# Performance work log

Hardware: AMD Instinct MI355X
Metric: run time of the kernel (lower is better)

Reference implementation:

```python
import jax, jax.numpy as jnp
import numpy as np

N_NODES = 50000
N_EDGES = 600000
D_FEAT = 128


def setup_inputs() -> dict:
    key = jax.random.key(0)
    k1, k2, k3 = jax.random.split(key, 3)
    x = jax.random.normal(k1, (N_NODES, D_FEAT), dtype=jnp.float32)
    edge_index = jax.random.randint(k2, (2, N_EDGES), 0, N_NODES, dtype=jnp.int64)
    line_graph_val = jax.random.normal(k3, (N_EDGES,), dtype=jnp.float32)  # unused by module
    return {"x": x, "edge_index": edge_index, "line_graph_val": line_graph_val}


def reference(x, edge_index, line_graph_val):
    # edge_index is unpacked as (j, i): j = source, i = target (GCN convention)
    src = edge_index[0]  # j
    dst = edge_index[1]  # i
    n = x.shape[0]
    # deg = scatter-add of ones over target indices i
    deg = jax.ops.segment_sum(jnp.ones_like(src, dtype=x.dtype), dst, num_segments=n)
    # deg^{-1/2}; guard deg==0 (torch would give inf; isolated targets have no edges anyway)
    deg_inv_sqrt = jnp.where(deg > 0, deg ** -0.5, jnp.zeros_like(deg))
    norm = deg_inv_sqrt[src] * deg_inv_sqrt[dst]  # [E]
    # spmm(edge_index[[1,0]], norm, n, n, x): out[i] += norm_e * x[j]
    msg = norm[:, None] * x[src]  # [E, F]
    out = jax.ops.segment_sum(msg, dst, num_segments=n)  # [N, F]
    return jax.nn.relu(out)
```

## Files before the change

kernel.cpp:

```cpp
#include <hip/hip_runtime.h>


#define SORTB    512
#define CHUNKMAX 1184
#define NBP      512
#define BCAP     2048

__device__ __forceinline__ int detect_is64(const unsigned int* w) {
    const int t = threadIdx.x & 63;
    unsigned long long m = __ballot(w[2 * t + 1] != 0u);
    return m == 0ull ? 1 : 0;
}

__device__ __forceinline__ int load_idx(const void* p, long long i, int is64) {
    return is64 ? (int)((const long long*)p)[i] : ((const int*)p)[i];
}

__device__ __forceinline__ unsigned short f2bf(float f) {
    unsigned u = __float_as_uint(f);
    unsigned r = (u + 0x7fffu + ((u >> 16) & 1u)) >> 16;
    return (unsigned short)r;
}

__global__ void k_zero_cur(int* cursor, int nb) {
    for (int i = threadIdx.x; i < nb; i += blockDim.x) cursor[i] = 0;
}

__global__ void __launch_bounds__(256) k_zero(int4* p, int n4) {
    const int stride = gridDim.x * blockDim.x;
    for (int i = blockIdx.x * blockDim.x + threadIdx.x; i < n4; i += stride)
        p[i] = make_int4(0, 0, 0, 0);
}


__global__ void __launch_bounds__(256) k_sort(const void* ei, int* cursor,
                                              unsigned int* __restrict__ buckets,
                                              int E, int CH) {
    __shared__ unsigned int raw[CHUNKMAX];
    __shared__ unsigned int srt[CHUNKMAX];
    __shared__ int hist[NBP];
    __shared__ int lbase[NBP];
    __shared__ int gbase[NBP];
    __shared__ int lcur[NBP];
    const int bid = blockIdx.x;
    const int t = threadIdx.x;
    for (int i = t; i < NBP; i += 256) hist[i] = 0;
    __syncthreads();
    const int is64 = detect_is64((const unsigned int*)ei);
    const int e0 = bid * CH;
    const int e1 = min(e0 + CH, E);
    const int nch = e1 - e0;
    for (int i = t; i < nch; i += 256) {
        const long long e = e0 + i;
        int s = load_idx(ei, e, is64);
        int d = load_idx(ei, (long long)E + e, is64);
        unsigned w = ((unsigned)d << 16) | (unsigned)s;
        raw[i] = w;
        atomicAdd(&hist[d >> 7], 1);
    }
    __syncthreads();
    if (t < 64) {
        const int base = t * 8;
        int v[8];
        int sum = 0;
        #pragma unroll
        for (int k = 0; k < 8; ++k) { v[k] = hist[base + k]; sum += v[k]; }
        int pre = sum;
        for (int off = 1; off < 64; off <<= 1) {
            int u = __shfl_up(pre, off);
            if (t >= off) pre += u;
        }
        pre -= sum;
        #pragma unroll
        for (int k = 0; k < 8; ++k) { lbase[base + k] = pre; pre += v[k]; }
    }
    __syncthreads();
    for (int b = t; b < NBP; b += 256) {
        const int c = hist[b];
        gbase[b] = c ? atomicAdd(&cursor[b], c) : 0;
        lcur[b] = lbase[b];
    }
    __syncthreads();
    for (int i = t; i < nch; i += 256) {
        const unsigned w = raw[i];
        const int p = atomicAdd(&lcur[w >> 23], 1);
        srt[p] = w;
    }
    __syncthreads();
    for (int i = t; i < nch; i += 256) {
        const unsigned w = srt[i];
        const int b = w >> 23;
        const int g = gbase[b] + (i - lbase[b]);
        if (g < BCAP) buckets[(size_t)b * BCAP + g] = w;
    }
}

__global__ void __launch_bounds__(256) k_finalize(const unsigned int* __restrict__ buckets,
                                                  const int* __restrict__ cursor,
                                                  const float* __restrict__ x,
                                                  unsigned short* __restrict__ xb,
                                                  unsigned short* __restrict__ srcs,
                                                  int2* __restrict__ seg, int n) {
    const int b = blockIdx.x;
    __shared__ unsigned int raw[BCAP];
    __shared__ unsigned short ss[BCAP];
    __shared__ int hist[128], base[128], lcur[128];
    __shared__ float sdinv[128];
    const int t = threadIdx.x;
    if (t < 128) hist[t] = 0;
    __syncthreads();
    const int len = min(cursor[b], BCAP);
    const unsigned int* bb = buckets + (size_t)b * BCAP;
    for (int i = t; i < len; i += 256) {
        const unsigned w = bb[i];
        raw[i] = w;
        atomicAdd(&hist[(w >> 16) & 127], 1);
    }
    __syncthreads();
    if (t < 64) {
        const int v0 = hist[2 * t], v1 = hist[2 * t + 1];
        const int sum = v0 + v1;
        int pre = sum;
        for (int off = 1; off < 64; off <<= 1) {
            int u = __shfl_up(pre, off);
            if (t >= off) pre += u;
        }
        pre -= sum;
        base[2 * t] = pre;          base[2 * t + 1] = pre + v0;
        lcur[2 * t] = pre;          lcur[2 * t + 1] = pre + v0;
    }
    __syncthreads();
    if (t < 128) {
        const int c = hist[t];
        sdinv[t] = (c > 0) ? rsqrtf((float)c) : 0.f;
        const int node = b * 128 + t;
        if (node < n)
            seg[node] = make_int2(b * BCAP + base[t], b * BCAP + base[t] + c);
    }
    __syncthreads();
    for (int i = t; i < len; i += 256) {
        const unsigned w = raw[i];
        const int p = atomicAdd(&lcur[(w >> 16) & 127], 1);
        ss[p] = (unsigned short)(w & 0xffffu);
    }
    __syncthreads();
    unsigned short* so = srcs + (size_t)b * BCAP;
    for (int i = t; i < len; i += 256) so[i] = ss[i];
    const long long rowbase = (long long)b * 128;
    #pragma unroll
    for (int j = 0; j < 8; ++j) {
        const int idx = j * 2048 + t * 8;
        const int r = idx >> 7;
        const int col = idx & 127;
        const long long node = rowbase + r;
        if (node < n) {
            const float w = sdinv[r];
            const float* xp = x + node * 128 + col;
            float4 a = *(const float4*)xp;
            float4 c4 = *(const float4*)(xp + 4);
            union { unsigned short us[8]; uint4 v; } o;
            o.us[0] = f2bf(w * a.x);  o.us[1] = f2bf(w * a.y);
            o.us[2] = f2bf(w * a.z);  o.us[3] = f2bf(w * a.w);
            o.us[4] = f2bf(w * c4.x); o.us[5] = f2bf(w * c4.y);
            o.us[6] = f2bf(w * c4.z); o.us[7] = f2bf(w * c4.w);
            *(uint4*)(xb + node * 128 + col) = o.v;
        }
    }
}

__global__ void __launch_bounds__(256) k_gather(const unsigned short* __restrict__ srcs,
                                                const int2* __restrict__ seg,
                                                const unsigned short* __restrict__ xb,
                                                float* __restrict__ out, int n) {
    const int node = blockIdx.x * 16 + (threadIdx.x >> 4);
    if (node >= n) return;
    const int lane = threadIdx.x & 15;
    const int2 sg = seg[node];
    int e = sg.x;
    const int eend = sg.y;
    const int deg = eend - e;
    float acc[8] = {0.f, 0.f, 0.f, 0.f, 0.f, 0.f, 0.f, 0.f};

    auto addv = [&](uint4 v) {
        acc[0] += __uint_as_float(v.x << 16);
        acc[1] += __uint_as_float(v.x & 0xffff0000u);
        acc[2] += __uint_as_float(v.y << 16);
        acc[3] += __uint_as_float(v.y & 0xffff0000u);
        acc[4] += __uint_as_float(v.z << 16);
        acc[5] += __uint_as_float(v.z & 0xffff0000u);
        acc[6] += __uint_as_float(v.w << 16);
        acc[7] += __uint_as_float(v.w & 0xffff0000u);
    };

    for (; e + 7 < eend; e += 8) {
        int s[8];
        uint4 v[8];
        #pragma unroll
        for (int k = 0; k < 8; ++k) s[k] = srcs[e + k];
        #pragma unroll
        for (int k = 0; k < 8; ++k) v[k] = ((const uint4*)(xb + (size_t)s[k] * 128))[lane];
        #pragma unroll
        for (int k = 0; k < 8; ++k) addv(v[k]);
    }
    for (; e + 1 < eend; e += 2) {
        const int s0 = srcs[e], s1 = srcs[e + 1];
        uint4 v0 = ((const uint4*)(xb + (size_t)s0 * 128))[lane];
        uint4 v1 = ((const uint4*)(xb + (size_t)s1 * 128))[lane];
        addv(v0); addv(v1);
    }
    if (e < eend) addv(((const uint4*)(xb + (size_t)srcs[e] * 128))[lane]);

    const float dd = (deg > 0) ? rsqrtf((float)deg) : 0.f;
    float4 o0, o1;
    o0.x = fmaxf(dd * acc[0], 0.f); o0.y = fmaxf(dd * acc[1], 0.f);
    o0.z = fmaxf(dd * acc[2], 0.f); o0.w = fmaxf(dd * acc[3], 0.f);
    o1.x = fmaxf(dd * acc[4], 0.f); o1.y = fmaxf(dd * acc[5], 0.f);
    o1.z = fmaxf(dd * acc[6], 0.f); o1.w = fmaxf(dd * acc[7], 0.f);
    float4* op = (float4*)(out + (size_t)node * 128);
    op[lane * 2] = o0;
    op[lane * 2 + 1] = o1;
}


__global__ void k_fill_direct(const void* ei, int* cnt, int* edges, int E, int cap) {
    const int is64 = detect_is64((const unsigned int*)ei);
    const int stride = gridDim.x * blockDim.x;
    for (int e = blockIdx.x * blockDim.x + threadIdx.x; e < E; e += stride) {
        int s = load_idx(ei, e, is64);
        int d = load_idx(ei, (long long)E + e, is64);
        int pos = atomicAdd(&cnt[d], 1);
        if (pos < cap) edges[(long long)d * cap + pos] = s;
    }
}

__global__ void __launch_bounds__(256) k_gather_pad(const float* __restrict__ x,
                                                    const int* __restrict__ edges,
                                                    const int* __restrict__ cnt,
                                                    float* __restrict__ out, int n, int cap) {
    const int node = blockIdx.x * 8 + (threadIdx.x >> 5);
    if (node >= n) return;
    const int lane = threadIdx.x & 31;
    const int m0 = cnt[node];
    const int m = min(m0, cap);
    const int* eb = edges + (long long)node * cap;
    float ax = 0.f, ay = 0.f, az = 0.f, aw = 0.f;
    int e = 0;
    for (; e + 3 < m; e += 4) {
        int s0 = eb[e], s1 = eb[e + 1], s2 = eb[e + 2], s3 = eb[e + 3];
        int c0 = cnt[s0], c1 = cnt[s1], c2 = cnt[s2], c3 = cnt[s3];
        float4 v0 = *(const float4*)(x + (long long)s0 * 128 + lane * 4);
        float4 v1 = *(const float4*)(x + (long long)s1 * 128 + lane * 4);
        float4 v2 = *(const float4*)(x + (long long)s2 * 128 + lane * 4);
        float4 v3 = *(const float4*)(x + (long long)s3 * 128 + lane * 4);
        float w0 = c0 > 0 ? rsqrtf((float)c0) : 0.f;
        float w1 = c1 > 0 ? rsqrtf((float)c1) : 0.f;
        float w2 = c2 > 0 ? rsqrtf((float)c2) : 0.f;
        float w3 = c3 > 0 ? rsqrtf((float)c3) : 0.f;
        ax += w0 * v0.x + w1 * v1.x + w2 * v2.x + w3 * v3.x;
        ay += w0 * v0.y + w1 * v1.y + w2 * v2.y + w3 * v3.y;
        az += w0 * v0.z + w1 * v1.z + w2 * v2.z + w3 * v3.z;
        aw += w0 * v0.w + w1 * v1.w + w2 * v2.w + w3 * v3.w;
    }
    for (; e < m; ++e) {
        int s0 = eb[e];
        int c0 = cnt[s0];
        float4 v0 = *(const float4*)(x + (long long)s0 * 128 + lane * 4);
        float w0 = c0 > 0 ? rsqrtf((float)c0) : 0.f;
        ax += w0 * v0.x; ay += w0 * v0.y; az += w0 * v0.z; aw += w0 * v0.w;
    }
    const float dd = m0 > 0 ? rsqrtf((float)m0) : 0.f;
    float4 rr;
    rr.x = fmaxf(dd * ax, 0.f); rr.y = fmaxf(dd * ay, 0.f);
    rr.z = fmaxf(dd * az, 0.f); rr.w = fmaxf(dd * aw, 0.f);
    *(float4*)(out + (long long)node * 128 + lane * 4) = rr;
}


__global__ void k_deg_simple(const void* ei, float* deg, int E) {
    const int is64 = detect_is64((const unsigned int*)ei);
    const int stride = gridDim.x * blockDim.x;
    for (int e = blockIdx.x * blockDim.x + threadIdx.x; e < E; e += stride)
        atomicAdd(&deg[load_idx(ei, (long long)E + e, is64)], 1.0f);
}
__global__ void k_dinv_simple(float* deg, int n) {
    int i = blockIdx.x * blockDim.x + threadIdx.x;
    if (i < n) { float d = deg[i]; deg[i] = d > 0.f ? rsqrtf(d) : 0.f; }
}
__global__ void k_scatter_atomic(const float* __restrict__ x, const void* ei,
                                 const float* __restrict__ dinv, float* out, int E) {
    const int is64 = detect_is64((const unsigned int*)ei);
    const int lane = threadIdx.x & 31;
    const int eslot = threadIdx.x >> 5;
    const int stride = gridDim.x * 8;
    for (int e = blockIdx.x * 8 + eslot; e < E; e += stride) {
        int s = load_idx(ei, e, is64);
        int d = load_idx(ei, (long long)E + e, is64);
        float norm = dinv[s] * dinv[d];
        float4 v = ((const float4*)(x + (long long)s * 128))[lane];
        float* o = out + (long long)d * 128 + lane * 4;
        atomicAdd(o + 0, norm * v.x); atomicAdd(o + 1, norm * v.y);
        atomicAdd(o + 2, norm * v.z); atomicAdd(o + 3, norm * v.w);
    }
}
__global__ void k_relu4(float4* out, int n4) {
    const int stride = gridDim.x * blockDim.x;
    for (int i = blockIdx.x * blockDim.x + threadIdx.x; i < n4; i += stride) {
        float4 v = out[i];
        v.x = fmaxf(v.x, 0.f); v.y = fmaxf(v.y, 0.f);
        v.z = fmaxf(v.z, 0.f); v.w = fmaxf(v.w, 0.f);
        out[i] = v;
    }
}

extern "C" void kernel_launch(void* const* d_in, const int* in_sizes, int n_in,
                              void* d_out, int out_size, void* d_ws, size_t ws_size,
                              hipStream_t stream) {
    const float* x = (const float*)d_in[0];
    const void* ei = d_in[1];
    const int D = 128;
    const int n = in_sizes[0] / D;
    const int E = in_sizes[1] / 2;

    char* ws = (char*)d_ws;
    size_t off = 0;
    auto alloc = [&](size_t bytes) {
        char* p = ws + off;
        off += (bytes + 255) & ~(size_t)255;
        return p;
    };
    auto al = [](size_t b) { return (b + 255) & ~(size_t)255; };

    const int nb = (n + 127) / 128;
    const int CH = (E + SORTB - 1) / SORTB;
    const size_t szCur = al((size_t)nb * 4);
    const size_t szBkt = al((size_t)nb * BCAP * 4);
    const size_t szSrc = al((size_t)nb * BCAP * 2);
    const size_t szSeg = al((size_t)n * 8);
    const size_t szXb  = al((size_t)n * D * 2);
    const size_t needS = szCur + szBkt + szSrc + szSeg + szXb;

    if (n <= 65536 && CH <= CHUNKMAX && nb <= NBP && ws_size >= needS) {
        int* cursor = (int*)alloc(szCur);
        unsigned int* buckets = (unsigned int*)alloc(szBkt);
        unsigned short* srcs = (unsigned short*)alloc(szSrc);
        int2* seg = (int2*)alloc(szSeg);
        unsigned short* xb = (unsigned short*)alloc(szXb);

        k_zero_cur<<<1, 512, 0, stream>>>(cursor, nb);
        k_sort<<<SORTB, 256, 0, stream>>>(ei, cursor, buckets, E, CH);
        k_finalize<<<nb, 256, 0, stream>>>(buckets, cursor, x, xb, srcs, seg, n);
        k_gather<<<(n + 15) / 16, 256, 0, stream>>>(srcs, seg, xb, (float*)d_out, n);
        return;
    }

    auto needD = [&](int c) { return al((size_t)n * 4) + al((size_t)n * c * 4); };
    if (ws_size >= needD(48)) {
        int c = (ws_size >= needD(64)) ? 64 : 48;
        int* cnt   = (int*)alloc((size_t)n * 4);
        int* edges = (int*)alloc((size_t)n * c * 4);
        k_zero<<<(n / 4 + 255) / 256, 256, 0, stream>>>((int4*)cnt, n / 4);
        k_fill_direct<<<2048, 256, 0, stream>>>(ei, cnt, edges, E, c);
        k_gather_pad<<<(n + 7) / 8, 256, 0, stream>>>(x, edges, cnt, (float*)d_out, n, c);
        return;
    }

    float* deg = (float*)alloc((size_t)n * 4);
    hipMemsetAsync(deg, 0, (size_t)n * sizeof(float), stream);
    hipMemsetAsync(d_out, 0, (size_t)out_size * sizeof(float), stream);
    k_deg_simple<<<2048, 256, 0, stream>>>(ei, deg, E);
    k_dinv_simple<<<(n + 255) / 256, 256, 0, stream>>>(deg, n);
    k_scatter_atomic<<<4096, 256, 0, stream>>>(x, ei, deg, (float*)d_out, E);
    k_relu4<<<2048, 256, 0, stream>>>((float4*)d_out, out_size / 4);
}
```

Measured before the change: 63.40 us.

## Overlap x-to-bf16 conversion with edge sort; apply src norm in gather

Moves the fp32-to-bf16 conversion of x out of the finalize kernel into extra blocks of the sort kernel, so it runs alongside the bucket sort instead of after it. Because the source degree is not known during the sort, the source normalisation is no longer folded into xb; finalize writes a per-node dinv array and the gather loads dinv[src] per edge and multiplies. Sort blocks are halved with larger chunks to make room. This adds one scalar load and FMA per edge in the gather and changes rounding slightly, since the unscaled value is now rounded to bf16.

Result: faster. 56.85 us (-10.3%).

```diff
diff --git a/kernel.cpp b/kernel.cpp
--- a/kernel.cpp
+++ b/kernel.cpp
@@ -1,8 +1,8 @@
 #include <hip/hip_runtime.h>
 
 
-#define SORTB    512
-#define CHUNKMAX 1184
+#define SORTB    256
+#define CHUNKMAX 2368
 #define NBP      512
 #define BCAP     2048
 
@@ -33,79 +33,92 @@
 }
 
 
-__global__ void __launch_bounds__(256) k_sort(const void* ei, int* cursor,
-                                              unsigned int* __restrict__ buckets,
-                                              int E, int CH) {
-    __shared__ unsigned int raw[CHUNKMAX];
-    __shared__ unsigned int srt[CHUNKMAX];
-    __shared__ int hist[NBP];
-    __shared__ int lbase[NBP];
-    __shared__ int gbase[NBP];
-    __shared__ int lcur[NBP];
+__global__ void __launch_bounds__(256) k_sort_conv(const void* ei, int* cursor,
+                                                   unsigned int* __restrict__ buckets,
+                                                   const float* __restrict__ x,
+                                                   unsigned short* __restrict__ xb,
+                                                   int E, int CH, int nconv) {
     const int bid = blockIdx.x;
-    const int t = threadIdx.x;
-    for (int i = t; i < NBP; i += 256) hist[i] = 0;
-    __syncthreads();
-    const int is64 = detect_is64((const unsigned int*)ei);
-    const int e0 = bid * CH;
-    const int e1 = min(e0 + CH, E);
-    const int nch = e1 - e0;
-    for (int i = t; i < nch; i += 256) {
-        const long long e = e0 + i;
-        int s = load_idx(ei, e, is64);
-        int d = load_idx(ei, (long long)E + e, is64);
-        unsigned w = ((unsigned)d << 16) | (unsigned)s;
-        raw[i] = w;
-        atomicAdd(&hist[d >> 7], 1);
-    }
-    __syncthreads();
-    if (t < 64) {
-        const int base = t * 8;
-        int v[8];
-        int sum = 0;
-        #pragma unroll
-        for (int k = 0; k < 8; ++k) { v[k] = hist[base + k]; sum += v[k]; }
-        int pre = sum;
-        for (int off = 1; off < 64; off <<= 1) {
-            int u = __shfl_up(pre, off);
-            if (t >= off) pre += u;
-        }
-        pre -= sum;
-        #pragma unroll
-        for (int k = 0; k < 8; ++k) { lbase[base + k] = pre; pre += v[k]; }
-    }
-    __syncthreads();
-    for (int b = t; b < NBP; b += 256) {
-        const int c = hist[b];
-        gbase[b] = c ? atomicAdd(&cursor[b], c) : 0;
-        lcur[b] = lbase[b];
-    }
-    __syncthreads();
-    for (int i = t; i < nch; i += 256) {
-        const unsigned w = raw[i];
-        const int p = atomicAdd(&lcur[w >> 23], 1);
-        srt[p] = w;
-    }
-    __syncthreads();
-    for (int i = t; i < nch; i += 256) {
-        const unsigned w = srt[i];
-        const int b = w >> 23;
-        const int g = gbase[b] + (i - lbase[b]);
-        if (g < BCAP) buckets[(size_t)b * BCAP + g] = w;
-    }
-}
-
-__global__ void __launch_bounds__(256) k_finalize(const unsigned int* __restrict__ buckets,
-                                                  const int* __restrict__ cursor,
-                                                  const float* __restrict__ x,
-                                                  unsigned short* __restrict__ xb,
-                                                  unsigned short* __restrict__ srcs,
-                                                  int2* __restrict__ seg, int n) {
+    if (bid < SORTB) {
+        __shared__ unsigned int raw[CHUNKMAX];
+        __shared__ unsigned int srt[CHUNKMAX];
+        __shared__ int hist[NBP];
+        __shared__ int lbase[NBP];
+        __shared__ int gbase[NBP];
+        __shared__ int lcur[NBP];
+        const int t = threadIdx.x;
+        for (int i = t; i < NBP; i += 256) hist[i] = 0;
+        __syncthreads();
+        const int is64 = detect_is64((const unsigned int*)ei);
+        const int e0 = bid * CH;
+        const int e1 = min(e0 + CH, E);
+        const int nch = e1 - e0;
+        for (int i = t; i < nch; i += 256) {
+            const long long e = e0 + i;
+            int s = load_idx(ei, e, is64);
+            int d = load_idx(ei, (long long)E + e, is64);
+            unsigned w = ((unsigned)d << 16) | (unsigned)s;
+            raw[i] = w;
+            atomicAdd(&hist[d >> 7], 1);
+        }
+        __syncthreads();
+        if (t < 64) {
+            const int base = t * 8;
+            int v[8];
+            int sum = 0;
+            #pragma unroll
+            for (int k = 0; k < 8; ++k) { v[k] = hist[base + k]; sum += v[k]; }
+            int pre = sum;
+            for (int off = 1; off < 64; off <<= 1) {
+                int u = __shfl_up(pre, off);
+                if (t >= off) pre += u;
+            }
+            pre -= sum;
+            #pragma unroll
+            for (int k = 0; k < 8; ++k) { lbase[base + k] = pre; pre += v[k]; }
+        }
+        __syncthreads();
+        for (int b = t; b < NBP; b += 256) {
+            const int c = hist[b];
+            gbase[b] = c ? atomicAdd(&cursor[b], c) : 0;
+            lcur[b] = lbase[b];
+        }
+        __syncthreads();
+        for (int i = t; i < nch; i += 256) {
+            const unsigned w = raw[i];
+            const int p = atomicAdd(&lcur[w >> 23], 1);
+            srt[p] = w;
+        }
+        __syncthreads();
+        for (int i = t; i < nch; i += 256) {
+            const unsigned w = srt[i];
+            const int b = w >> 23;
+            const int g = gbase[b] + (i - lbase[b]);
+            if (g < BCAP) buckets[(size_t)b * BCAP + g] = w;
+        }
+    } else if (xb) {
+        const long long tid = (long long)(bid - SORTB) * 256 + threadIdx.x;
+        if (tid < nconv) {
+            const long long i = tid * 8;
+            float4 a = *(const float4*)(x + i);
+            float4 b = *(const float4*)(x + i + 4);
+            union { unsigned short us[8]; uint4 v; } o;
+            o.us[0] = f2bf(a.x); o.us[1] = f2bf(a.y); o.us[2] = f2bf(a.z); o.us[3] = f2bf(a.w);
+            o.us[4] = f2bf(b.x); o.us[5] = f2bf(b.y); o.us[6] = f2bf(b.z); o.us[7] = f2bf(b.w);
+            *(uint4*)(xb + i) = o.v;
+        }
+    }
+}
+
+__global__ void __launch_bounds__(256) k_finseg(const unsigned int* __restrict__ buckets,
+                                                const int* __restrict__ cursor,
+                                                unsigned short* __restrict__ srcs,
+                                                int2* __restrict__ seg,
+                                                float* __restrict__ dinv, int n) {
     const int b = blockIdx.x;
     __shared__ unsigned int raw[BCAP];
     __shared__ unsigned short ss[BCAP];
     __shared__ int hist[128], base[128], lcur[128];
-    __shared__ float sdinv[128];
     const int t = threadIdx.x;
     if (t < 128) hist[t] = 0;
     __syncthreads();
@@ -126,16 +139,17 @@
             if (t >= off) pre += u;
         }
         pre -= sum;
-        base[2 * t] = pre;          base[2 * t + 1] = pre + v0;
-        lcur[2 * t] = pre;          lcur[2 * t + 1] = pre + v0;
+        base[2 * t] = pre;  base[2 * t + 1] = pre + v0;
+        lcur[2 * t] = pre;  lcur[2 * t + 1] = pre + v0;
     }
     __syncthreads();
     if (t < 128) {
-        const int c = hist[t];
-        sdinv[t] = (c > 0) ? rsqrtf((float)c) : 0.f;
         const int node = b * 128 + t;
-        if (node < n)
+        if (node < n) {
+            const int c = hist[t];
             seg[node] = make_int2(b * BCAP + base[t], b * BCAP + base[t] + c);
+            dinv[node] = (c > 0) ? rsqrtf((float)c) : 0.f;
+        }
     }
     __syncthreads();
     for (int i = t; i < len; i += 256) {
@@ -146,31 +160,12 @@
     __syncthreads();
     unsigned short* so = srcs + (size_t)b * BCAP;
     for (int i = t; i < len; i += 256) so[i] = ss[i];
-    const long long rowbase = (long long)b * 128;
-    #pragma unroll
-    for (int j = 0; j < 8; ++j) {
-        const int idx = j * 2048 + t * 8;
-        const int r = idx >> 7;
-        const int col = idx & 127;
-        const long long node = rowbase + r;
-        if (node < n) {
-            const float w = sdinv[r];
-            const float* xp = x + node * 128 + col;
-            float4 a = *(const float4*)xp;
-            float4 c4 = *(const float4*)(xp + 4);
-            union { unsigned short us[8]; uint4 v; } o;
-            o.us[0] = f2bf(w * a.x);  o.us[1] = f2bf(w * a.y);
-            o.us[2] = f2bf(w * a.z);  o.us[3] = f2bf(w * a.w);
-            o.us[4] = f2bf(w * c4.x); o.us[5] = f2bf(w * c4.y);
-            o.us[6] = f2bf(w * c4.z); o.us[7] = f2bf(w * c4.w);
-            *(uint4*)(xb + node * 128 + col) = o.v;
-        }
-    }
 }
 
 __global__ void __launch_bounds__(256) k_gather(const unsigned short* __restrict__ srcs,
                                                 const int2* __restrict__ seg,
                                                 const unsigned short* __restrict__ xb,
+                                                const float* __restrict__ dinv,
                                                 float* __restrict__ out, int n) {
     const int node = blockIdx.x * 16 + (threadIdx.x >> 4);
     if (node >= n) return;
@@ -181,34 +176,41 @@
     const int deg = eend - e;
     float acc[8] = {0.f, 0.f, 0.f, 0.f, 0.f, 0.f, 0.f, 0.f};
 
-    auto addv = [&](uint4 v) {
-        acc[0] += __uint_as_float(v.x << 16);
-        acc[1] += __uint_as_float(v.x & 0xffff0000u);
-        acc[2] += __uint_as_float(v.y << 16);
-        acc[3] += __uint_as_float(v.y & 0xffff0000u);
-        acc[4] += __uint_as_float(v.z << 16);
-        acc[5] += __uint_as_float(v.z & 0xffff0000u);
-        acc[6] += __uint_as_float(v.w << 16);
-        acc[7] += __uint_as_float(v.w & 0xffff0000u);
+    auto addv = [&](uint4 v, float w) {
+        acc[0] += w * __uint_as_float(v.x << 16);
+        acc[1] += w * __uint_as_float(v.x & 0xffff0000u);
+        acc[2] += w * __uint_as_float(v.y << 16);
+        acc[3] += w * __uint_as_float(v.y & 0xffff0000u);
+        acc[4] += w * __uint_as_float(v.z << 16);
+        acc[5] += w * __uint_as_float(v.z & 0xffff0000u);
+        acc[6] += w * __uint_as_float(v.w << 16);
+        acc[7] += w * __uint_as_float(v.w & 0xffff0000u);
     };
 
     for (; e + 7 < eend; e += 8) {
         int s[8];
+        float w[8];
         uint4 v[8];
         #pragma unroll
         for (int k = 0; k < 8; ++k) s[k] = srcs[e + k];
         #pragma unroll
+        for (int k = 0; k < 8; ++k) w[k] = dinv[s[k]];
+        #pragma unroll
         for (int k = 0; k < 8; ++k) v[k] = ((const uint4*)(xb + (size_t)s[k] * 128))[lane];
         #pragma unroll
-        for (int k = 0; k < 8; ++k) addv(v[k]);
+        for (int k = 0; k < 8; ++k) addv(v[k], w[k]);
     }
     for (; e + 1 < eend; e += 2) {
         const int s0 = srcs[e], s1 = srcs[e + 1];
+        const float w0 = dinv[s0], w1 = dinv[s1];
         uint4 v0 = ((const uint4*)(xb + (size_t)s0 * 128))[lane];
         uint4 v1 = ((const uint4*)(xb + (size_t)s1 * 128))[lane];
-        addv(v0); addv(v1);
-    }
-    if (e < eend) addv(((const uint4*)(xb + (size_t)srcs[e] * 128))[lane]);
+        addv(v0, w0); addv(v1, w1);
+    }
+    if (e < eend) {
+        const int s0 = srcs[e];
+        addv(((const uint4*)(xb + (size_t)s0 * 128))[lane], dinv[s0]);
+    }
 
     const float dd = (deg > 0) ? rsqrtf((float)deg) : 0.f;
     float4 o0, o1;
@@ -336,20 +338,24 @@
     const size_t szBkt = al((size_t)nb * BCAP * 4);
     const size_t szSrc = al((size_t)nb * BCAP * 2);
     const size_t szSeg = al((size_t)n * 8);
+    const size_t szDnv = al((size_t)n * 4);
     const size_t szXb  = al((size_t)n * D * 2);
-    const size_t needS = szCur + szBkt + szSrc + szSeg + szXb;
+    const size_t needS = szCur + szBkt + szSrc + szSeg + szDnv + szXb;
 
     if (n <= 65536 && CH <= CHUNKMAX && nb <= NBP && ws_size >= needS) {
         int* cursor = (int*)alloc(szCur);
         unsigned int* buckets = (unsigned int*)alloc(szBkt);
         unsigned short* srcs = (unsigned short*)alloc(szSrc);
         int2* seg = (int2*)alloc(szSeg);
+        float* dinv = (float*)alloc(szDnv);
         unsigned short* xb = (unsigned short*)alloc(szXb);
 
         k_zero_cur<<<1, 512, 0, stream>>>(cursor, nb);
-        k_sort<<<SORTB, 256, 0, stream>>>(ei, cursor, buckets, E, CH);
-        k_finalize<<<nb, 256, 0, stream>>>(buckets, cursor, x, xb, srcs, seg, n);
-        k_gather<<<(n + 15) / 16, 256, 0, stream>>>(srcs, seg, xb, (float*)d_out, n);
+        const int nconv = n * D / 8;
+        const int grid1 = SORTB + (nconv + 255) / 256;
+        k_sort_conv<<<grid1, 256, 0, stream>>>(ei, cursor, buckets, x, xb, E, CH, nconv);
+        k_finseg<<<nb, 256, 0, stream>>>(buckets, cursor, srcs, seg, dinv, n);
+        k_gather<<<(n + 15) / 16, 256, 0, stream>>>(srcs, seg, xb, dinv, (float*)d_out, n);
         return;
     }
 
```
